# Performance work log

Measured on AMD Instinct MI355X. Metric: run time of the kernel, lower is better.

Reference implementation:

```python
import jax, jax.numpy as jnp
import numpy as np

DIM = 1024; HEADS = 16; HEAD = 64; FFN_H = 4096
LE = 8; TOPK = 2; DIM_E = 512; DIM_S = 1024
B = 1; S = 2048; N = B * S; NMOE = 2
THETA = 10000.0; EPS = 1e-6; RSF = 1.0


def rmsnorm(x, g):
    return x * jax.lax.rsqrt(jnp.mean(x * x, axis=-1, keepdims=True) + EPS) * g


def rotary(x):
    # x: [b, h, s, a]; matches RotaryEmb: split halves, y1=x1*cos+x2*sin, y2=-x1*sin+x2*cos
    a = x.shape[-1]; s = x.shape[2]
    inv_freq = (1.0 / THETA) ** (jnp.arange(0, a, 2, dtype=jnp.float32) / a)
    freqs = jnp.arange(s, dtype=jnp.float32)[:, None] * inv_freq[None, :]  # [s, a/2]
    cos, sin = jnp.cos(freqs), jnp.sin(freqs)
    x1, x2 = jnp.split(x, 2, axis=-1)
    return jnp.concatenate([x1 * cos + x2 * sin, -x1 * sin + x2 * cos], axis=-1)


def attention(x, attn_w, attn_o, doc):
    # causal + same-document masked attention (flex_attention mask_mod equivalent)
    b, s, d = x.shape
    xq, xk, xv = jnp.split(x @ attn_w, 3, axis=-1)
    def heads(t):
        return t.reshape(b, s, HEADS, HEAD).transpose(0, 2, 1, 3)
    xq, xk, xv = heads(xq), heads(xk), heads(xv)
    xq, xk = rotary(xq), rotary(xk)
    scores = jnp.einsum('bhqa,bhka->bhqk', xq, xk) / jnp.sqrt(jnp.float32(HEAD))
    q_idx = jnp.arange(s)
    mask = (q_idx[:, None] >= q_idx[None, :])[None] & (doc[:, :, None] == doc[:, None, :])
    scores = jnp.where(mask[:, None, :, :], scores, -jnp.inf)
    probs = jax.nn.softmax(scores, axis=-1)
    out = jnp.einsum('bhqk,bhka->bhqa', probs, xv)
    return out.transpose(0, 2, 1, 3).reshape(b, s, d) @ attn_o


def dense_layer(x, aw, ao, up, down, ag, fg, doc):
    xi = attention(rmsnorm(x, ag), aw, ao, doc) + x
    xf = rmsnorm(xi, fg)
    x1, x2 = jnp.split(xf @ up, 2, axis=-1)
    return (jax.nn.silu(x1) * x2) @ down + xi


def moe_layer(x, aw, ao, ag, fg, experts, tkeys, rbias, sup, sdown, idx, vals, doc):
    xi = attention(rmsnorm(x, ag), aw, ao, doc) + x
    xf = rmsnorm(xi, fg)                     # [b,s,d]
    flat = xf.reshape(-1, DIM)               # [N,d]
    # routing: base values + token-key logits + bias, sigmoid, renormalize
    tv = flat @ tkeys                        # [N,le]
    vals = vals + jnp.take_along_axis(tv, idx, axis=-1) + rbias[idx]
    sc = jax.nn.sigmoid(vals)
    sc = sc / jnp.sum(sc, axis=-1, keepdims=True) * RSF   # [N,k]
    # grouped-gemm experts (SwiGLU per expert); dense-over-experts then gather
    h1 = jnp.einsum('nd,edh->neh', flat, experts[0])
    h2 = jnp.einsum('nd,edh->neh', flat, experts[1])
    y_all = jnp.einsum('neh,edh->ned', jax.nn.silu(h1) * h2, experts[2])
    y_sel = jnp.take_along_axis(y_all, idx[:, :, None], axis=1)   # [N,k,d]
    y = jnp.sum(y_sel * sc[:, :, None], axis=1).reshape(xf.shape)
    # shared expert
    x1, x2 = jnp.split(xf @ sup, 2, axis=-1)
    y = y + (jax.nn.silu(x1) * x2) @ sdown
    return y + xi


def setup_inputs() -> dict:
    key = jax.random.key(0)
    ks = jax.random.split(key, 24)
    w = lambda k, shp: (jax.random.normal(k, shp, dtype=jnp.float32) * 0.02)
    inp = {
        'x': jax.random.normal(ks[0], (B, S, DIM), dtype=jnp.float32),
        'doc': jnp.sort(jax.random.randint(ks[1], (B, S), 0, 4), axis=-1).astype(jnp.int32),
        'indices': jax.random.randint(ks[2], (NMOE, N, TOPK), 0, LE).astype(jnp.int64),
        'values': jax.random.normal(ks[3], (NMOE, N, TOPK), dtype=jnp.float32),
        # 2 dense layers (first_k=1, last_k=1)
        'dense_attn_w': w(ks[4], (2, DIM, 3 * DIM)),
        'dense_attn_o': w(ks[5], (2, DIM, DIM)),
        'dense_ffn_up': w(ks[6], (2, DIM, 2 * FFN_H)),
        'dense_ffn_down': w(ks[7], (2, FFN_H, DIM)),
        'dense_attn_g': jnp.ones((2, DIM), dtype=jnp.float32),
        'dense_ffn_g': jnp.ones((2, DIM), dtype=jnp.float32),
        # 2 MoE layers
        'moe_attn_w': w(ks[8], (NMOE, DIM, 3 * DIM)),
        'moe_attn_o': w(ks[9], (NMOE, DIM, DIM)),
        'moe_attn_g': jnp.ones((NMOE, DIM), dtype=jnp.float32),
        'moe_ffn_g': jnp.ones((NMOE, DIM), dtype=jnp.float32),
        'moe_experts': w(ks[10], (NMOE, 3, LE, DIM, DIM_E)),
        'moe_token_keys': w(ks[11], (NMOE, DIM, LE)),
        'moe_router_bias': jnp.zeros((NMOE, LE), dtype=jnp.float32),
        'moe_shared_up': w(ks[12], (NMOE, DIM, 2 * DIM_S)),
        'moe_shared_down': w(ks[13], (NMOE, DIM_S, DIM)),
    }
    return inp


def reference(x, doc, indices, values, dense_attn_w, dense_attn_o, dense_ffn_up,
              dense_ffn_down, dense_attn_g, dense_ffn_g, moe_attn_w, moe_attn_o,
              moe_attn_g, moe_ffn_g, moe_experts, moe_token_keys, moe_router_bias,
              moe_shared_up, moe_shared_down):
    x = dense_layer(x, dense_attn_w[0], dense_attn_o[0], dense_ffn_up[0],
                    dense_ffn_down[0], dense_attn_g[0], dense_ffn_g[0], doc)
    for i in range(NMOE):
        x = moe_layer(x, moe_attn_w[i], moe_attn_o[i], moe_attn_g[i], moe_ffn_g[i],
                      moe_experts[i], moe_token_keys[i], moe_router_bias[i],
                      moe_shared_up[i], moe_shared_down[i], indices[i], values[i], doc)
    x = dense_layer(x, dense_attn_w[1], dense_attn_o[1], dense_ffn_up[1],
                    dense_ffn_down[1], dense_attn_g[1], dense_ffn_g[1], doc)
    return x
```

## Files before the change

kernel.cpp:

```cpp
#include <hip/hip_runtime.h>
#include <cmath>
#include <cstddef>
#include <cstdint>

#define DIMM   1024
#define HEADS  16
#define HEADD  64
#define FFN_H  4096
#define LE     8
#define TOPK   2
#define DIM_E  512
#define DIM_S  1024
#define NTOK   2048

typedef __bf16 bf16x8 __attribute__((ext_vector_type(8)));
typedef float  f32x4  __attribute__((ext_vector_type(4)));

union BF4 { __bf16 h[4]; uint2 u; };
union BF2 { __bf16 h[2]; uint32_t u; };

__device__ __forceinline__ void ldg_lds16(const __bf16* g, __bf16* l) {
    __builtin_amdgcn_global_load_lds(
        (const __attribute__((address_space(1))) uint32_t*)g,
        (__attribute__((address_space(3))) uint32_t*)l, 16, 0, 0);
}

__global__ __launch_bounds__(256) void rmsnorm_bf(
    const float* __restrict__ x, const float* __restrict__ g,
    __bf16* __restrict__ y)
{
    const int row = blockIdx.x;
    const int t = threadIdx.x;
    const float* xr = x + (size_t)row * DIMM;
    float4 v = *(const float4*)(xr + t * 4);
    float ss = v.x * v.x + v.y * v.y + v.z * v.z + v.w * v.w;
    #pragma unroll
    for (int off = 32; off > 0; off >>= 1) ss += __shfl_down(ss, off, 64);
    __shared__ float ws[4];
    if ((t & 63) == 0) ws[t >> 6] = ss;
    __syncthreads();
    const float tot = ws[0] + ws[1] + ws[2] + ws[3];
    const float scale = rsqrtf(tot * (1.0f / DIMM) + 1e-6f);
    const float4 gv = *(const float4*)(g + t * 4);
    BF4 o;
    o.h[0] = (__bf16)(v.x * scale * gv.x);
    o.h[1] = (__bf16)(v.y * scale * gv.y);
    o.h[2] = (__bf16)(v.z * scale * gv.z);
    o.h[3] = (__bf16)(v.w * scale * gv.w);
    *(uint2*)(y + (size_t)row * DIMM + t * 4) = o.u;
}

template <typename OutT>
__global__ __launch_bounds__(256) void gemm_bf_t(
    const __bf16* __restrict__ A, const __bf16* __restrict__ BT,
    const float* __restrict__ add, OutT* __restrict__ C,
    int M, int N, int K)
{
    __shared__ __bf16 As[128 * 32];
    __shared__ __bf16 Bs[128 * 32];
    const int t = threadIdx.x;
    const int m0 = blockIdx.y * 128, n0 = blockIdx.x * 128;
    const int lane = t & 63;
    const int wv = t >> 6;
    const int mw = (wv >> 1) * 64, nw = (wv & 1) * 64;
    const int fr = lane & 15;
    const int fk = (lane >> 4) * 8;
    const int r0 = t >> 2;
    const int q0 = (t & 3) * 8;

    const __bf16* gA0 = A + (size_t)(m0 + r0) * K + q0;
    const __bf16* gA1 = A + (size_t)(m0 + 64 + r0) * K + q0;
    const __bf16* gB0 = BT + (size_t)(n0 + r0) * K + q0;
    const __bf16* gB1 = BT + (size_t)(n0 + 64 + r0) * K + q0;
    __bf16* lA0 = &As[r0 * 32 + q0];
    __bf16* lA1 = &As[(64 + r0) * 32 + q0];
    __bf16* lB0 = &Bs[r0 * 32 + q0];
    __bf16* lB1 = &Bs[(64 + r0) * 32 + q0];

    f32x4 acc[4][4];
    #pragma unroll
    for (int i = 0; i < 4; ++i)
        #pragma unroll
        for (int j = 0; j < 4; ++j) acc[i][j] = (f32x4){0.f, 0.f, 0.f, 0.f};

    for (int k0 = 0; k0 < K; k0 += 32) {
        __syncthreads();
        ldg_lds16(gA0 + k0, lA0);
        ldg_lds16(gA1 + k0, lA1);
        ldg_lds16(gB0 + k0, lB0);
        ldg_lds16(gB1 + k0, lB1);
        __syncthreads();
        bf16x8 af[4], bfr[4];
        #pragma unroll
        for (int i = 0; i < 4; ++i) {
            af[i]  = *(const bf16x8*)&As[(mw + i * 16 + fr) * 32 + fk];
            bfr[i] = *(const bf16x8*)&Bs[(nw + i * 16 + fr) * 32 + fk];
        }
        #pragma unroll
        for (int i = 0; i < 4; ++i)
            #pragma unroll
            for (int j = 0; j < 4; ++j)
                acc[i][j] = __builtin_amdgcn_mfma_f32_16x16x32_bf16(
                    af[i], bfr[j], acc[i][j], 0, 0, 0);
    }
    const int cn = lane & 15, cr = (lane >> 4) * 4;
    #pragma unroll
    for (int i = 0; i < 4; ++i)
        #pragma unroll
        for (int j = 0; j < 4; ++j)
            #pragma unroll
            for (int r = 0; r < 4; ++r) {
                const size_t off = (size_t)(m0 + mw + i * 16 + cr + r) * N
                                 + (n0 + nw + j * 16 + cn);
                if constexpr (__is_same(OutT, float))
                    C[off] = acc[i][j][r] + (add ? add[off] : 0.f);
                else
                    C[off] = (__bf16)acc[i][j][r];
            }
}

__global__ __launch_bounds__(256) void gemm_bf_splitk(
    const __bf16* __restrict__ A, const __bf16* __restrict__ BT,
    float* __restrict__ P, int M, int N, int K, int KS)
{
    __shared__ __bf16 As[128 * 32];
    __shared__ __bf16 Bs[128 * 32];
    const int t = threadIdx.x;
    const int m0 = blockIdx.y * 128, n0 = blockIdx.x * 128;
    const int kz0 = blockIdx.z * KS;
    const int lane = t & 63;
    const int wv = t >> 6;
    const int mw = (wv >> 1) * 64, nw = (wv & 1) * 64;
    const int fr = lane & 15;
    const int fk = (lane >> 4) * 8;
    const int r0 = t >> 2;
    const int q0 = (t & 3) * 8;

    const __bf16* gA0 = A + (size_t)(m0 + r0) * K + q0;
    const __bf16* gA1 = A + (size_t)(m0 + 64 + r0) * K + q0;
    const __bf16* gB0 = BT + (size_t)(n0 + r0) * K + q0;
    const __bf16* gB1 = BT + (size_t)(n0 + 64 + r0) * K + q0;
    __bf16* lA0 = &As[r0 * 32 + q0];
    __bf16* lA1 = &As[(64 + r0) * 32 + q0];
    __bf16* lB0 = &Bs[r0 * 32 + q0];
    __bf16* lB1 = &Bs[(64 + r0) * 32 + q0];

    f32x4 acc[4][4];
    #pragma unroll
    for (int i = 0; i < 4; ++i)
        #pragma unroll
        for (int j = 0; j < 4; ++j) acc[i][j] = (f32x4){0.f, 0.f, 0.f, 0.f};

    for (int k0 = kz0; k0 < kz0 + KS; k0 += 32) {
        __syncthreads();
        ldg_lds16(gA0 + k0, lA0);
        ldg_lds16(gA1 + k0, lA1);
        ldg_lds16(gB0 + k0, lB0);
        ldg_lds16(gB1 + k0, lB1);
        __syncthreads();
        bf16x8 af[4], bfr[4];
        #pragma unroll
        for (int i = 0; i < 4; ++i) {
            af[i]  = *(const bf16x8*)&As[(mw + i * 16 + fr) * 32 + fk];
            bfr[i] = *(const bf16x8*)&Bs[(nw + i * 16 + fr) * 32 + fk];
        }
        #pragma unroll
        for (int i = 0; i < 4; ++i)
            #pragma unroll
            for (int j = 0; j < 4; ++j)
                acc[i][j] = __builtin_amdgcn_mfma_f32_16x16x32_bf16(
                    af[i], bfr[j], acc[i][j], 0, 0, 0);
    }
    float* Pz = P + (size_t)blockIdx.z * M * N;
    const int cn = lane & 15, cr = (lane >> 4) * 4;
    #pragma unroll
    for (int i = 0; i < 4; ++i)
        #pragma unroll
        for (int j = 0; j < 4; ++j)
            #pragma unroll
            for (int r = 0; r < 4; ++r) {
                const size_t off = (size_t)(m0 + mw + i * 16 + cr + r) * N
                                 + (n0 + nw + j * 16 + cn);
                Pz[off] = acc[i][j][r];
            }
}

__global__ __launch_bounds__(256) void reduce4_add(
    const float* __restrict__ P, const float* __restrict__ add,
    float* __restrict__ out, size_t MN)
{
    const size_t i = ((size_t)blockIdx.x * 256 + threadIdx.x) * 4;
    float4 s  = *(const float4*)(P + i);
    const float4 s1 = *(const float4*)(P + MN + i);
    const float4 s2 = *(const float4*)(P + 2 * MN + i);
    const float4 s3 = *(const float4*)(P + 3 * MN + i);
    const float4 a  = *(const float4*)(add + i);
    s.x += s1.x + s2.x + s3.x + a.x;
    s.y += s1.y + s2.y + s3.y + a.y;
    s.z += s1.z + s2.z + s3.z + a.z;
    s.w += s1.w + s2.w + s3.w + a.w;
    *(float4*)(out + i) = s;
}

__global__ __launch_bounds__(256) void transpose_cast(
    const float* __restrict__ in, __bf16* __restrict__ out, int R, int C)
{
    __shared__ float tile[32][33];
    const int bx = blockIdx.x * 32, by = blockIdx.y * 32;
    const size_t bz = (size_t)blockIdx.z * R * C;
    const int tx = threadIdx.x & 31, ty = threadIdx.x >> 5;
    const float* ip = in + bz;
    __bf16* op = out + bz;
    #pragma unroll
    for (int i = 0; i < 4; ++i)
        tile[ty + i * 8][tx] = ip[(size_t)(by + ty + i * 8) * C + bx + tx];
    __syncthreads();
    #pragma unroll
    for (int i = 0; i < 4; ++i)
        op[(size_t)(bx + ty + i * 8) * R + by + tx] = (__bf16)tile[tx][ty + i * 8];
}

__global__ __launch_bounds__(256) void cast_w2(
    const float* __restrict__ in, __bf16* __restrict__ out)
{
    const int i = blockIdx.x * 256 + threadIdx.x;
    const int d = i >> 12, r = i & 4095;
    const int e = r >> 9, h = r & 511;
    out[i] = (__bf16)in[(size_t)e * (DIMM * DIM_E) + d * DIM_E + h];
}

__global__ __launch_bounds__(256) void rotary_kernel(float* __restrict__ qkv)
{
    const int i = blockIdx.x * 256 + threadIdx.x;
    const int s = i >> 9;
    const int rem = i & 511;
    const int h = rem >> 5;
    const int j = rem & 31;
    const float inv_freq = __expf(-(float)j * (9.210340371976184f / 32.f));
    const float f = (float)s * inv_freq;
    float sn, cs;
    sincosf(f, &sn, &cs);
    float* base = qkv + (size_t)s * 3072 + h * 64 + j;
    const float q1 = base[0], q2 = base[32];
    base[0]  = q1 * cs + q2 * sn;
    base[32] = -q1 * sn + q2 * cs;
    const float k1 = base[1024], k2 = base[1024 + 32];
    base[1024]      = k1 * cs + k2 * sn;
    base[1024 + 32] = -k1 * sn + k2 * cs;
}

#define KS_STRIDE 72
#define VT_STRIDE 72
#define PW_STRIDE 36
#define LOG2E 1.4426950408889634f

__global__ __launch_bounds__(256) void attn_mfma(
    const float* __restrict__ qkv, const int* __restrict__ doc,
    __bf16* __restrict__ out)
{
    const int h = blockIdx.x;
    const int qb = blockIdx.y;
    const int t = threadIdx.x;
    const int wv = t >> 6, lane = t & 63;
    const int l15 = lane & 15, lhi = lane >> 4;
    const int q0w = qb * 64 + wv * 16;

    __shared__ __bf16 Ks[64 * KS_STRIDE];
    __shared__ __bf16 Vt[64 * VT_STRIDE];
    __shared__ float  Pw[4][16 * PW_STRIDE];
    __shared__ int    docs[64];

    bf16x8 qf[2];
    {
        const float* qrow = qkv + (size_t)(q0w + l15) * 3072 + h * 64 + lhi * 8;
        #pragma unroll
        for (int db = 0; db < 2; ++db) {
            const float4 v0 = *(const float4*)(qrow + db * 32);
            const float4 v1 = *(const float4*)(qrow + db * 32 + 4);
            bf16x8 f;
            f[0] = (__bf16)(v0.x * 0.125f); f[1] = (__bf16)(v0.y * 0.125f);
            f[2] = (__bf16)(v0.z * 0.125f); f[3] = (__bf16)(v0.w * 0.125f);
            f[4] = (__bf16)(v1.x * 0.125f); f[5] = (__bf16)(v1.y * 0.125f);
            f[6] = (__bf16)(v1.z * 0.125f); f[7] = (__bf16)(v1.w * 0.125f);
            qf[db] = f;
        }
    }
    int myDoc[4];
    #pragma unroll
    for (int rg = 0; rg < 4; ++rg) myDoc[rg] = doc[q0w + lhi * 4 + rg];

    float mrow[4] = {-INFINITY, -INFINITY, -INFINITY, -INFINITY};
    float lrow[4] = {0.f, 0.f, 0.f, 0.f};
    f32x4 oacc[4];
    #pragma unroll
    for (int nb = 0; nb < 4; ++nb) oacc[nb] = (f32x4){0.f, 0.f, 0.f, 0.f};

    const int docQ0 = doc[qb * 64];
    const int ntiles = qb + 1;

    for (int kt = 0; kt < ntiles; ++kt) {
        if (doc[kt * 64 + 63] < docQ0) continue;
        __syncthreads();
        {
            const int key = t >> 2, dof = (t & 3) * 16;
            const float* kr = qkv + (size_t)(kt * 64 + key) * 3072 + 1024 + h * 64 + dof;
            float kv[16];
            *(float4*)&kv[0]  = *(const float4*)(kr + 0);
            *(float4*)&kv[4]  = *(const float4*)(kr + 4);
            *(float4*)&kv[8]  = *(const float4*)(kr + 8);
            *(float4*)&kv[12] = *(const float4*)(kr + 12);
            bf16x8 p0, p1;
            #pragma unroll
            for (int j = 0; j < 8; ++j) { p0[j] = (__bf16)kv[j]; p1[j] = (__bf16)kv[8 + j]; }
            *(bf16x8*)&Ks[key * KS_STRIDE + dof] = p0;
            *(bf16x8*)&Ks[key * KS_STRIDE + dof + 8] = p1;
            const int k2 = (t & 31) * 2, df = (t >> 5) * 8;
            const float* vr0 = qkv + (size_t)(kt * 64 + k2) * 3072 + 2048 + h * 64 + df;
            float va[8], vb[8];
            *(float4*)&va[0] = *(const float4*)(vr0 + 0);
            *(float4*)&va[4] = *(const float4*)(vr0 + 4);
            *(float4*)&vb[0] = *(const float4*)(vr0 + 3072);
            *(float4*)&vb[4] = *(const float4*)(vr0 + 3076);
            #pragma unroll
            for (int d = 0; d < 8; ++d) {
                BF2 wpk;
                wpk.h[0] = (__bf16)va[d];
                wpk.h[1] = (__bf16)vb[d];
                *(uint32_t*)&Vt[(df + d) * VT_STRIDE + k2] = wpk.u;
            }
            if (t < 64) docs[t] = doc[kt * 64 + t];
        }
        __syncthreads();

        #pragma unroll
        for (int g = 0; g < 2; ++g) {
            f32x4 s[2];
            #pragma unroll
            for (int sg = 0; sg < 2; ++sg) {
                const int keyloc = g * 32 + sg * 16;
                const bf16x8 kf0 = *(const bf16x8*)&Ks[(keyloc + l15) * KS_STRIDE + lhi * 8];
                const bf16x8 kf1 = *(const bf16x8*)&Ks[(keyloc + l15) * KS_STRIDE + 32 + lhi * 8];
                f32x4 a = (f32x4){0.f, 0.f, 0.f, 0.f};
                a = __builtin_amdgcn_mfma_f32_16x16x32_bf16(qf[0], kf0, a, 0, 0, 0);
                a = __builtin_amdgcn_mfma_f32_16x16x32_bf16(qf[1], kf1, a, 0, 0, 0);
                s[sg] = a;
            }
            float sv0[4], sv1[4], cmax[4];
            #pragma unroll
            for (int rg = 0; rg < 4; ++rg) {
                const int r = q0w + lhi * 4 + rg;
                const int key0 = kt * 64 + g * 32 + l15;
                const bool v0 = (key0 <= r) && (docs[g * 32 + l15] == myDoc[rg]);
                const bool v1 = (key0 + 16 <= r) && (docs[g * 32 + 16 + l15] == myDoc[rg]);
                sv0[rg] = v0 ? s[0][rg] : -INFINITY;
                sv1[rg] = v1 ? s[1][rg] : -INFINITY;
                cmax[rg] = fmaxf(sv0[rg], sv1[rg]);
            }
            #pragma unroll
            for (int off = 1; off < 16; off <<= 1)
                #pragma unroll
                for (int rg = 0; rg < 4; ++rg)
                    cmax[rg] = fmaxf(cmax[rg], __shfl_xor(cmax[rg], off, 64));
            float alpha[4], p0[4], p1[4], rsum[4];
            #pragma unroll
            for (int rg = 0; rg < 4; ++rg) {
                const float mn = fmaxf(mrow[rg], cmax[rg]);
                alpha[rg] = (mn == -INFINITY) ? 1.f : exp2f((mrow[rg] - mn) * LOG2E);
                p0[rg] = (sv0[rg] == -INFINITY) ? 0.f : exp2f((sv0[rg] - mn) * LOG2E);
                p1[rg] = (sv1[rg] == -INFINITY) ? 0.f : exp2f((sv1[rg] - mn) * LOG2E);
                rsum[rg] = p0[rg] + p1[rg];
                mrow[rg] = mn;
            }
            #pragma unroll
            for (int off = 1; off < 16; off <<= 1)
                #pragma unroll
                for (int rg = 0; rg < 4; ++rg)
                    rsum[rg] += __shfl_xor(rsum[rg], off, 64);
            #pragma unroll
            for (int rg = 0; rg < 4; ++rg)
                lrow[rg] = lrow[rg] * alpha[rg] + rsum[rg];
            #pragma unroll
            for (int nb = 0; nb < 4; ++nb)
                #pragma unroll
                for (int rg = 0; rg < 4; ++rg)
                    oacc[nb][rg] *= alpha[rg];
            float* pp = &Pw[wv][0];
            #pragma unroll
            for (int rg = 0; rg < 4; ++rg) {
                pp[(lhi * 4 + rg) * PW_STRIDE + l15] = p0[rg];
                pp[(lhi * 4 + rg) * PW_STRIDE + 16 + l15] = p1[rg];
            }
            const f32x4 pa = *(const f32x4*)&pp[l15 * PW_STRIDE + lhi * 8];
            const f32x4 pb = *(const f32x4*)&pp[l15 * PW_STRIDE + lhi * 8 + 4];
            bf16x8 pf;
            pf[0] = (__bf16)pa[0]; pf[1] = (__bf16)pa[1];
            pf[2] = (__bf16)pa[2]; pf[3] = (__bf16)pa[3];
            pf[4] = (__bf16)pb[0]; pf[5] = (__bf16)pb[1];
            pf[6] = (__bf16)pb[2]; pf[7] = (__bf16)pb[3];
            #pragma unroll
            for (int nb = 0; nb < 4; ++nb) {
                const bf16x8 vf = *(const bf16x8*)&Vt[(nb * 16 + l15) * VT_STRIDE + g * 32 + lhi * 8];
                oacc[nb] = __builtin_amdgcn_mfma_f32_16x16x32_bf16(pf, vf, oacc[nb], 0, 0, 0);
            }
        }
    }
    float inv[4];
    #pragma unroll
    for (int rg = 0; rg < 4; ++rg) inv[rg] = 1.f / lrow[rg];
    #pragma unroll
    for (int nb = 0; nb < 4; ++nb)
        #pragma unroll
        for (int rg = 0; rg < 4; ++rg)
            out[(size_t)(q0w + lhi * 4 + rg) * DIMM + h * 64 + nb * 16 + l15] =
                (__bf16)(oacc[nb][rg] * inv[rg]);
}

__global__ __launch_bounds__(256) void swiglu_bf2(
    const __bf16* __restrict__ h, __bf16* __restrict__ g, int shift)
{
    const int i4 = blockIdx.x * 256 + threadIdx.x;
    const int H = 1 << shift;
    const int n = (i4 * 4) >> shift;
    const int j = (i4 * 4) & (H - 1);
    const __bf16* hr = h + ((size_t)n << (shift + 1));
    BF4 a, b;
    a.u = *(const uint2*)(hr + j);
    b.u = *(const uint2*)(hr + H + j);
    BF4 o;
    #pragma unroll
    for (int u = 0; u < 4; ++u) {
        const float av = (float)a.h[u], bv = (float)b.h[u];
        o.h[u] = (__bf16)((av / (1.f + __expf(-av))) * bv);
    }
    *(uint2*)(g + (size_t)i4 * 4) = o.u;
}

__global__ __launch_bounds__(256) void pmask_bf2(
    const __bf16* __restrict__ hh, const float* __restrict__ sc,
    __bf16* __restrict__ p)
{
    const int i4 = blockIdx.x * 256 + threadIdx.x;
    const int n = i4 >> 10;
    const int j4 = i4 & 1023;
    const int e = j4 >> 7;
    const float s = sc[n * LE + e];
    const __bf16* hr = hh + (size_t)n * 8192 + j4 * 4;
    BF4 a, b;
    a.u = *(const uint2*)(hr);
    b.u = *(const uint2*)(hr + 4096);
    BF4 o;
    #pragma unroll
    for (int u = 0; u < 4; ++u) {
        const float av = (float)a.h[u], bv = (float)b.h[u];
        o.h[u] = (__bf16)((av / (1.f + __expf(-av))) * bv * s);
    }
    *(uint2*)(p + (size_t)i4 * 4) = o.u;
}

__global__ __launch_bounds__(64) void router_bf(
    const __bf16* __restrict__ xf, const float* __restrict__ tkeys,
    const float* __restrict__ rbias, const int* __restrict__ idx,
    const float* __restrict__ vals, float* __restrict__ sc)
{
    const int n = blockIdx.x;
    const int t = threadIdx.x;
    const int e0 = idx[n * 2 + 0], e1 = idx[n * 2 + 1];
    float a0 = 0.f, a1 = 0.f;
    for (int d = t; d < DIMM; d += 64) {
        const float xv = (float)xf[(size_t)n * DIMM + d];
        a0 += xv * tkeys[d * LE + e0];
        a1 += xv * tkeys[d * LE + e1];
    }
    #pragma unroll
    for (int off = 32; off > 0; off >>= 1) {
        a0 += __shfl_down(a0, off, 64);
        a1 += __shfl_down(a1, off, 64);
    }
    if (t == 0) {
        const float v0 = vals[n * 2 + 0] + a0 + rbias[e0];
        const float v1 = vals[n * 2 + 1] + a1 + rbias[e1];
        const float s0 = 1.f / (1.f + __expf(-v0));
        const float s1 = 1.f / (1.f + __expf(-v1));
        const float inv = 1.f / (s0 + s1);
        float r[LE];
        #pragma unroll
        for (int e = 0; e < LE; ++e) r[e] = 0.f;
        r[e0] += s0 * inv;
        r[e1] += s1 * inv;
        #pragma unroll
        for (int e = 0; e < LE; ++e) sc[n * LE + e] = r[e];
    }
}

struct Scratch {
    float *qkv, *xi, *t1, *sc, *xA, *xB, *part;
    __bf16 *xn_bf, *attnO_bf, *xf_bf, *wbuf, *gact_bf, *gs_bf, *hh_bf, *hs_bf;
};

static void attn_block(const float* x_in, const __bf16* awT, const __bf16* aoT,
                       const float* ag, const int* doc, Scratch& w, hipStream_t s)
{
    rmsnorm_bf<<<NTOK, 256, 0, s>>>(x_in, ag, w.xn_bf);
    gemm_bf_t<float><<<dim3(24, 16), 256, 0, s>>>(w.xn_bf, awT, nullptr, w.qkv, NTOK, 3072, 1024);
    rotary_kernel<<<(NTOK * 512) / 256, 256, 0, s>>>(w.qkv);
    attn_mfma<<<dim3(HEADS, NTOK / 64), 256, 0, s>>>(w.qkv, doc, w.attnO_bf);
    gemm_bf_t<float><<<dim3(8, 16), 256, 0, s>>>(w.attnO_bf, aoT, x_in, w.xi, NTOK, 1024, 1024);
}

static void dense_layer_run(const float* x_in, float* x_out,
                            const float* aw, const float* ao,
                            const float* up, const float* down,
                            const float* ag, const float* fg,
                            const int* doc, Scratch& w, hipStream_t s)
{
    __bf16* awT = w.wbuf;
    __bf16* aoT = w.wbuf + 3145728;
    __bf16* upT = w.wbuf + 4194304;
    __bf16* dnT = w.wbuf + 12582912;
    transpose_cast<<<dim3(96, 32, 1), 256, 0, s>>>(aw, awT, 1024, 3072);
    transpose_cast<<<dim3(32, 32, 1), 256, 0, s>>>(ao, aoT, 1024, 1024);
    transpose_cast<<<dim3(256, 32, 1), 256, 0, s>>>(up, upT, 1024, 8192);
    transpose_cast<<<dim3(32, 128, 1), 256, 0, s>>>(down, dnT, 4096, 1024);
    attn_block(x_in, awT, aoT, ag, doc, w, s);
    rmsnorm_bf<<<NTOK, 256, 0, s>>>(w.xi, fg, w.xf_bf);
    gemm_bf_t<__bf16><<<dim3(64, 16), 256, 0, s>>>(w.xf_bf, upT, nullptr, w.hh_bf, NTOK, 8192, 1024);
    swiglu_bf2<<<(NTOK * FFN_H / 4) / 256, 256, 0, s>>>(w.hh_bf, w.gact_bf, 12);
    gemm_bf_splitk<<<dim3(8, 16, 4), 256, 0, s>>>(w.gact_bf, dnT, w.part, NTOK, 1024, 4096, 1024);
    reduce4_add<<<(NTOK * 1024) / 1024, 256, 0, s>>>(w.part, w.xi, x_out, (size_t)NTOK * 1024);
}

static void moe_layer_run(const float* x_in, float* x_out,
                          const float* aw, const float* ao,
                          const float* ag, const float* fg,
                          const float* experts, const float* tkeys,
                          const float* rbias, const float* sup,
                          const float* sdn, const int* idx, const float* vals,
                          const int* doc, Scratch& w, hipStream_t s)
{
    __bf16* awT  = w.wbuf;
    __bf16* aoT  = w.wbuf + 3145728;
    __bf16* w01T = w.wbuf + 4194304;
    __bf16* w2c  = w.wbuf + 12582912;
    __bf16* supT = w.wbuf + 16777216;
    __bf16* sdnT = w.wbuf + 18874368;
    const size_t EW = (size_t)LE * DIMM * DIM_E;
    transpose_cast<<<dim3(96, 32, 1), 256, 0, s>>>(aw, awT, 1024, 3072);
    transpose_cast<<<dim3(32, 32, 1), 256, 0, s>>>(ao, aoT, 1024, 1024);
    transpose_cast<<<dim3(16, 32, 8), 256, 0, s>>>(experts, w01T, 1024, 512);
    transpose_cast<<<dim3(16, 32, 8), 256, 0, s>>>(experts + EW, w01T + 4194304, 1024, 512);
    cast_w2<<<16384, 256, 0, s>>>(experts + 2 * EW, w2c);
    transpose_cast<<<dim3(64, 32, 1), 256, 0, s>>>(sup, supT, 1024, 2048);
    transpose_cast<<<dim3(32, 32, 1), 256, 0, s>>>(sdn, sdnT, 1024, 1024);

    attn_block(x_in, awT, aoT, ag, doc, w, s);
    rmsnorm_bf<<<NTOK, 256, 0, s>>>(w.xi, fg, w.xf_bf);
    router_bf<<<NTOK, 64, 0, s>>>(w.xf_bf, tkeys, rbias, idx, vals, w.sc);
    gemm_bf_t<__bf16><<<dim3(64, 16), 256, 0, s>>>(w.xf_bf, w01T, nullptr, w.hh_bf, NTOK, 8192, 1024);
    pmask_bf2<<<(NTOK * 4096 / 4) / 256, 256, 0, s>>>(w.hh_bf, w.sc, w.gact_bf);
    gemm_bf_t<__bf16><<<dim3(16, 16), 256, 0, s>>>(w.xf_bf, supT, nullptr, w.hs_bf, NTOK, 2048, 1024);
    swiglu_bf2<<<(NTOK * DIM_S / 4) / 256, 256, 0, s>>>(w.hs_bf, w.gs_bf, 10);
    gemm_bf_t<float><<<dim3(8, 16), 256, 0, s>>>(w.gs_bf, sdnT, w.xi, w.t1, NTOK, 1024, 1024);
    gemm_bf_splitk<<<dim3(8, 16, 4), 256, 0, s>>>(w.gact_bf, w2c, w.part, NTOK, 1024, 4096, 1024);
    reduce4_add<<<(NTOK * 1024) / 1024, 256, 0, s>>>(w.part, w.t1, x_out, (size_t)NTOK * 1024);
}

extern "C" void kernel_launch(void* const* d_in, const int* in_sizes, int n_in,
                              void* d_out, int out_size, void* d_ws, size_t ws_size,
                              hipStream_t stream)
{
    (void)in_sizes; (void)n_in; (void)out_size; (void)ws_size;
    const float* x       = (const float*)d_in[0];
    const int*   doc     = (const int*)d_in[1];
    const int*   indices = (const int*)d_in[2];
    const float* values  = (const float*)d_in[3];
    const float* d_aw    = (const float*)d_in[4];
    const float* d_ao    = (const float*)d_in[5];
    const float* d_up    = (const float*)d_in[6];
    const float* d_down  = (const float*)d_in[7];
    const float* d_ag    = (const float*)d_in[8];
    const float* d_fg    = (const float*)d_in[9];
    const float* m_aw    = (const float*)d_in[10];
    const float* m_ao    = (const float*)d_in[11];
    const float* m_ag    = (const float*)d_in[12];
    const float* m_fg    = (const float*)d_in[13];
    const float* m_ex    = (const float*)d_in[14];
    const float* m_tk    = (const float*)d_in[15];
    const float* m_rb    = (const float*)d_in[16];
    const float* m_sup   = (const float*)d_in[17];
    const float* m_sdn   = (const float*)d_in[18];

    Scratch w;
    float* f = (float*)d_ws;
    w.qkv = f; f += 6291456;
    w.xi  = f; f += 2097152;
    float* h12 = f; f += 16777216;
    w.t1  = h12 + 8388608;
    w.sc  = f; f += 16384;
    w.xA  = f; f += 2097152;
    w.xB  = f; f += 2097152;
    __bf16* b = (__bf16*)f;
    w.xn_bf    = b; b += 2097152;
    w.attnO_bf = b; b += 2097152;
    w.xf_bf    = b; b += 2097152;
    w.wbuf     = b; b += 19922944;
    w.gact_bf  = (__bf16*)w.qkv;
    w.gs_bf    = (__bf16*)w.qkv + 8388608;
    w.hh_bf    = (__bf16*)h12;
    w.hs_bf    = (__bf16*)(h12 + 8388608 + 2097152);
    w.part     = h12;

    float* out = (float*)d_out;

    dense_layer_run(x, w.xA, d_aw, d_ao, d_up, d_down, d_ag, d_fg, doc, w, stream);
    const size_t EXL = (size_t)3 * LE * DIMM * DIM_E;
    moe_layer_run(w.xA, w.xB,
                  m_aw, m_ao, m_ag, m_fg,
                  m_ex, m_tk, m_rb, m_sup, m_sdn,
                  indices, values, doc, w, stream);
    moe_layer_run(w.xB, w.xA,
                  m_aw + (size_t)DIMM * 3 * DIMM, m_ao + (size_t)DIMM * DIMM,
                  m_ag + DIMM, m_fg + DIMM,
                  m_ex + EXL, m_tk + DIMM * LE, m_rb + LE,
                  m_sup + (size_t)DIMM * 2 * DIM_S, m_sdn + (size_t)DIM_S * DIMM,
                  indices + (size_t)NTOK * TOPK, values + (size_t)NTOK * TOPK,
                  doc, w, stream);
    dense_layer_run(w.xA, out,
                    d_aw + (size_t)DIMM * 3 * DIMM, d_ao + (size_t)DIMM * DIMM,
                    d_up + (size_t)DIMM * 2 * FFN_H, d_down + (size_t)FFN_H * DIMM,
                    d_ag + DIMM, d_fg + DIMM, doc, w, stream);
}
```

Baseline: 1.437 ms.

## Fuse SwiGLU into up-projection GEMM, swizzle LDS, split-K small GEMMs

Adds a gemm_glu kernel that loads paired gate/up weight rows into one tile and applies SiLU-gate (and router scale) in the epilogue, removing the separate swiglu/pmask passes and the intermediate bf16 hidden buffers. GEMM kernels get an XOR swizzle on LDS columns to reduce bank conflicts on fragment reads. The N=1024,K=1024 output projections switch to 2-way split-K plus a reduce kernel to raise block count. This adds an extra fp32 partial buffer round trip for those GEMMs.

```diff
diff --git a/kernel.cpp b/kernel.cpp
--- a/kernel.cpp
+++ b/kernel.cpp
@@ -64,18 +64,19 @@
     const int wv = t >> 6;
     const int mw = (wv >> 1) * 64, nw = (wv & 1) * 64;
     const int fr = lane & 15;
-    const int fk = (lane >> 4) * 8;
+    const int fk = ((lane >> 4) ^ ((fr >> 1) & 3)) * 8;
     const int r0 = t >> 2;
-    const int q0 = (t & 3) * 8;
-
-    const __bf16* gA0 = A + (size_t)(m0 + r0) * K + q0;
-    const __bf16* gA1 = A + (size_t)(m0 + 64 + r0) * K + q0;
-    const __bf16* gB0 = BT + (size_t)(n0 + r0) * K + q0;
-    const __bf16* gB1 = BT + (size_t)(n0 + 64 + r0) * K + q0;
-    __bf16* lA0 = &As[r0 * 32 + q0];
-    __bf16* lA1 = &As[(64 + r0) * 32 + q0];
-    __bf16* lB0 = &Bs[r0 * 32 + q0];
-    __bf16* lB1 = &Bs[(64 + r0) * 32 + q0];
+    const int q0l = (t & 3) * 8;
+    const int q0s = ((t & 3) ^ ((t >> 3) & 3)) * 8;
+
+    const __bf16* gA0 = A + (size_t)(m0 + r0) * K + q0s;
+    const __bf16* gA1 = A + (size_t)(m0 + 64 + r0) * K + q0s;
+    const __bf16* gB0 = BT + (size_t)(n0 + r0) * K + q0s;
+    const __bf16* gB1 = BT + (size_t)(n0 + 64 + r0) * K + q0s;
+    __bf16* lA0 = &As[r0 * 32 + q0l];
+    __bf16* lA1 = &As[(64 + r0) * 32 + q0l];
+    __bf16* lB0 = &Bs[r0 * 32 + q0l];
+    __bf16* lB1 = &Bs[(64 + r0) * 32 + q0l];
 
     f32x4 acc[4][4];
     #pragma unroll
@@ -132,18 +133,19 @@
     const int wv = t >> 6;
     const int mw = (wv >> 1) * 64, nw = (wv & 1) * 64;
     const int fr = lane & 15;
-    const int fk = (lane >> 4) * 8;
+    const int fk = ((lane >> 4) ^ ((fr >> 1) & 3)) * 8;
     const int r0 = t >> 2;
-    const int q0 = (t & 3) * 8;
-
-    const __bf16* gA0 = A + (size_t)(m0 + r0) * K + q0;
-    const __bf16* gA1 = A + (size_t)(m0 + 64 + r0) * K + q0;
-    const __bf16* gB0 = BT + (size_t)(n0 + r0) * K + q0;
-    const __bf16* gB1 = BT + (size_t)(n0 + 64 + r0) * K + q0;
-    __bf16* lA0 = &As[r0 * 32 + q0];
-    __bf16* lA1 = &As[(64 + r0) * 32 + q0];
-    __bf16* lB0 = &Bs[r0 * 32 + q0];
-    __bf16* lB1 = &Bs[(64 + r0) * 32 + q0];
+    const int q0l = (t & 3) * 8;
+    const int q0s = ((t & 3) ^ ((t >> 3) & 3)) * 8;
+
+    const __bf16* gA0 = A + (size_t)(m0 + r0) * K + q0s;
+    const __bf16* gA1 = A + (size_t)(m0 + 64 + r0) * K + q0s;
+    const __bf16* gB0 = BT + (size_t)(n0 + r0) * K + q0s;
+    const __bf16* gB1 = BT + (size_t)(n0 + 64 + r0) * K + q0s;
+    __bf16* lA0 = &As[r0 * 32 + q0l];
+    __bf16* lA1 = &As[(64 + r0) * 32 + q0l];
+    __bf16* lB0 = &Bs[r0 * 32 + q0l];
+    __bf16* lB1 = &Bs[(64 + r0) * 32 + q0l];
 
     f32x4 acc[4][4];
     #pragma unroll
@@ -183,6 +185,83 @@
                                  + (n0 + nw + j * 16 + cn);
                 Pz[off] = acc[i][j][r];
             }
+}
+
+__global__ __launch_bounds__(256) void gemm_glu(
+    const __bf16* __restrict__ A, const __bf16* __restrict__ BT,
+    const float* __restrict__ sc, __bf16* __restrict__ G,
+    int M, int Nout, int K, int pairOff)
+{
+    __shared__ __bf16 As[128 * 32];
+    __shared__ __bf16 Bs[128 * 32];
+    const int t = threadIdx.x;
+    const int m0 = blockIdx.y * 128;
+    const int b  = blockIdx.x;
+    const int lane = t & 63;
+    const int wv = t >> 6;
+    const int mw = (wv >> 1) * 64, nw = (wv & 1) * 64;
+    const int fr = lane & 15;
+    const int fk = ((lane >> 4) ^ ((fr >> 1) & 3)) * 8;
+    const int r0 = t >> 2;
+    const int q0l = (t & 3) * 8;
+    const int q0s = ((t & 3) ^ ((t >> 3) & 3)) * 8;
+
+    const int grow0 = b * 64 + ((r0 >> 6) ? 32 : 0) + (r0 & 31)
+                    + ((r0 >> 5) & 1) * pairOff;
+    const int grow1 = grow0 + 32;
+
+    const __bf16* gA0 = A + (size_t)(m0 + r0) * K + q0s;
+    const __bf16* gA1 = A + (size_t)(m0 + 64 + r0) * K + q0s;
+    const __bf16* gB0 = BT + (size_t)grow0 * K + q0s;
+    const __bf16* gB1 = BT + (size_t)grow1 * K + q0s;
+    __bf16* lA0 = &As[r0 * 32 + q0l];
+    __bf16* lA1 = &As[(64 + r0) * 32 + q0l];
+    __bf16* lB0 = &Bs[r0 * 32 + q0l];
+    __bf16* lB1 = &Bs[(64 + r0) * 32 + q0l];
+
+    f32x4 acc[4][4];
+    #pragma unroll
+    for (int i = 0; i < 4; ++i)
+        #pragma unroll
+        for (int j = 0; j < 4; ++j) acc[i][j] = (f32x4){0.f, 0.f, 0.f, 0.f};
+
+    for (int k0 = 0; k0 < K; k0 += 32) {
+        __syncthreads();
+        ldg_lds16(gA0 + k0, lA0);
+        ldg_lds16(gA1 + k0, lA1);
+        ldg_lds16(gB0 + k0, lB0);
+        ldg_lds16(gB1 + k0, lB1);
+        __syncthreads();
+        bf16x8 af[4], bfr[4];
+        #pragma unroll
+        for (int i = 0; i < 4; ++i) {
+            af[i]  = *(const bf16x8*)&As[(mw + i * 16 + fr) * 32 + fk];
+            bfr[i] = *(const bf16x8*)&Bs[(nw + i * 16 + fr) * 32 + fk];
+        }
+        #pragma unroll
+        for (int i = 0; i < 4; ++i)
+            #pragma unroll
+            for (int j = 0; j < 4; ++j)
+                acc[i][j] = __builtin_amdgcn_mfma_f32_16x16x32_bf16(
+                    af[i], bfr[j], acc[i][j], 0, 0, 0);
+    }
+    const int cn = lane & 15, cr = (lane >> 4) * 4;
+    const int e = (b * 64) >> 9;
+    #pragma unroll
+    for (int i = 0; i < 4; ++i)
+        #pragma unroll
+        for (int r = 0; r < 4; ++r) {
+            const int m = m0 + mw + i * 16 + cr + r;
+            const float s = sc ? sc[m * LE + e] : 1.f;
+            #pragma unroll
+            for (int j = 0; j < 2; ++j) {
+                const float h1 = acc[i][j][r];
+                const float h2 = acc[i][j + 2][r];
+                const float o = (h1 / (1.f + __expf(-h1))) * h2 * s;
+                const int col = b * 64 + (nw >> 1) + j * 16 + cn;
+                G[(size_t)m * Nout + col] = (__bf16)o;
+            }
+        }
 }
 
 __global__ __launch_bounds__(256) void reduce4_add(
@@ -199,6 +278,21 @@
     s.y += s1.y + s2.y + s3.y + a.y;
     s.z += s1.z + s2.z + s3.z + a.z;
     s.w += s1.w + s2.w + s3.w + a.w;
+    *(float4*)(out + i) = s;
+}
+
+__global__ __launch_bounds__(256) void reduce2_add(
+    const float* __restrict__ P, const float* __restrict__ add,
+    float* __restrict__ out, size_t MN)
+{
+    const size_t i = ((size_t)blockIdx.x * 256 + threadIdx.x) * 4;
+    float4 s  = *(const float4*)(P + i);
+    const float4 s1 = *(const float4*)(P + MN + i);
+    const float4 a  = *(const float4*)(add + i);
+    s.x += s1.x + a.x;
+    s.y += s1.y + a.y;
+    s.z += s1.z + a.z;
+    s.w += s1.w + a.w;
     *(float4*)(out + i) = s;
 }
 
@@ -415,48 +509,6 @@
                 (__bf16)(oacc[nb][rg] * inv[rg]);
 }
 
-__global__ __launch_bounds__(256) void swiglu_bf2(
-    const __bf16* __restrict__ h, __bf16* __restrict__ g, int shift)
-{
-    const int i4 = blockIdx.x * 256 + threadIdx.x;
-    const int H = 1 << shift;
-    const int n = (i4 * 4) >> shift;
-    const int j = (i4 * 4) & (H - 1);
-    const __bf16* hr = h + ((size_t)n << (shift + 1));
-    BF4 a, b;
-    a.u = *(const uint2*)(hr + j);
-    b.u = *(const uint2*)(hr + H + j);
-    BF4 o;
-    #pragma unroll
-    for (int u = 0; u < 4; ++u) {
-        const float av = (float)a.h[u], bv = (float)b.h[u];
-        o.h[u] = (__bf16)((av / (1.f + __expf(-av))) * bv);
-    }
-    *(uint2*)(g + (size_t)i4 * 4) = o.u;
-}
-
-__global__ __launch_bounds__(256) void pmask_bf2(
-    const __bf16* __restrict__ hh, const float* __restrict__ sc,
-    __bf16* __restrict__ p)
-{
-    const int i4 = blockIdx.x * 256 + threadIdx.x;
-    const int n = i4 >> 10;
-    const int j4 = i4 & 1023;
-    const int e = j4 >> 7;
-    const float s = sc[n * LE + e];
-    const __bf16* hr = hh + (size_t)n * 8192 + j4 * 4;
-    BF4 a, b;
-    a.u = *(const uint2*)(hr);
-    b.u = *(const uint2*)(hr + 4096);
-    BF4 o;
-    #pragma unroll
-    for (int u = 0; u < 4; ++u) {
-        const float av = (float)a.h[u], bv = (float)b.h[u];
-        o.h[u] = (__bf16)((av / (1.f + __expf(-av))) * bv * s);
-    }
-    *(uint2*)(p + (size_t)i4 * 4) = o.u;
-}
-
 __global__ __launch_bounds__(64) void router_bf(
     const __bf16* __restrict__ xf, const float* __restrict__ tkeys,
     const float* __restrict__ rbias, const int* __restrict__ idx,
@@ -494,7 +546,7 @@
 
 struct Scratch {
     float *qkv, *xi, *t1, *sc, *xA, *xB, *part;
-    __bf16 *xn_bf, *attnO_bf, *xf_bf, *wbuf, *gact_bf, *gs_bf, *hh_bf, *hs_bf;
+    __bf16 *xn_bf, *attnO_bf, *xf_bf, *wbuf, *gact_bf, *gs_bf;
 };
 
 static void attn_block(const float* x_in, const __bf16* awT, const __bf16* aoT,
@@ -504,7 +556,8 @@
     gemm_bf_t<float><<<dim3(24, 16), 256, 0, s>>>(w.xn_bf, awT, nullptr, w.qkv, NTOK, 3072, 1024);
     rotary_kernel<<<(NTOK * 512) / 256, 256, 0, s>>>(w.qkv);
     attn_mfma<<<dim3(HEADS, NTOK / 64), 256, 0, s>>>(w.qkv, doc, w.attnO_bf);
-    gemm_bf_t<float><<<dim3(8, 16), 256, 0, s>>>(w.attnO_bf, aoT, x_in, w.xi, NTOK, 1024, 1024);
+    gemm_bf_splitk<<<dim3(8, 16, 2), 256, 0, s>>>(w.attnO_bf, aoT, w.qkv, NTOK, 1024, 1024, 512);
+    reduce2_add<<<(NTOK * 1024) / 1024, 256, 0, s>>>(w.qkv, x_in, w.xi, (size_t)NTOK * 1024);
 }
 
 static void dense_layer_run(const float* x_in, float* x_out,
@@ -523,8 +576,7 @@
     transpose_cast<<<dim3(32, 128, 1), 256, 0, s>>>(down, dnT, 4096, 1024);
     attn_block(x_in, awT, aoT, ag, doc, w, s);
     rmsnorm_bf<<<NTOK, 256, 0, s>>>(w.xi, fg, w.xf_bf);
-    gemm_bf_t<__bf16><<<dim3(64, 16), 256, 0, s>>>(w.xf_bf, upT, nullptr, w.hh_bf, NTOK, 8192, 1024);
-    swiglu_bf2<<<(NTOK * FFN_H / 4) / 256, 256, 0, s>>>(w.hh_bf, w.gact_bf, 12);
+    gemm_glu<<<dim3(64, 16), 256, 0, s>>>(w.xf_bf, upT, nullptr, w.gact_bf, NTOK, 4096, 1024, 4096);
     gemm_bf_splitk<<<dim3(8, 16, 4), 256, 0, s>>>(w.gact_bf, dnT, w.part, NTOK, 1024, 4096, 1024);
     reduce4_add<<<(NTOK * 1024) / 1024, 256, 0, s>>>(w.part, w.xi, x_out, (size_t)NTOK * 1024);
 }
@@ -555,11 +607,10 @@
     attn_block(x_in, awT, aoT, ag, doc, w, s);
     rmsnorm_bf<<<NTOK, 256, 0, s>>>(w.xi, fg, w.xf_bf);
     router_bf<<<NTOK, 64, 0, s>>>(w.xf_bf, tkeys, rbias, idx, vals, w.sc);
-    gemm_bf_t<__bf16><<<dim3(64, 16), 256, 0, s>>>(w.xf_bf, w01T, nullptr, w.hh_bf, NTOK, 8192, 1024);
-    pmask_bf2<<<(NTOK * 4096 / 4) / 256, 256, 0, s>>>(w.hh_bf, w.sc, w.gact_bf);
-    gemm_bf_t<__bf16><<<dim3(16, 16), 256, 0, s>>>(w.xf_bf, supT, nullptr, w.hs_bf, NTOK, 2048, 1024);
-    swiglu_bf2<<<(NTOK * DIM_S / 4) / 256, 256, 0, s>>>(w.hs_bf, w.gs_bf, 10);
-    gemm_bf_t<float><<<dim3(8, 16), 256, 0, s>>>(w.gs_bf, sdnT, w.xi, w.t1, NTOK, 1024, 1024);
+    gemm_glu<<<dim3(64, 16), 256, 0, s>>>(w.xf_bf, w01T, w.sc, w.gact_bf, NTOK, 4096, 1024, 4096);
+    gemm_glu<<<dim3(16, 16), 256, 0, s>>>(w.xf_bf, supT, nullptr, w.gs_bf, NTOK, 1024, 1024, 1024);
+    gemm_bf_splitk<<<dim3(8, 16, 2), 256, 0, s>>>(w.gs_bf, sdnT, w.part, NTOK, 1024, 1024, 512);
+    reduce2_add<<<(NTOK * 1024) / 1024, 256, 0, s>>>(w.part, w.xi, w.t1, (size_t)NTOK * 1024);
     gemm_bf_splitk<<<dim3(8, 16, 4), 256, 0, s>>>(w.gact_bf, w2c, w.part, NTOK, 1024, 4096, 1024);
     reduce4_add<<<(NTOK * 1024) / 1024, 256, 0, s>>>(w.part, w.t1, x_out, (size_t)NTOK * 1024);
 }
@@ -605,8 +656,6 @@
     w.wbuf     = b; b += 19922944;
     w.gact_bf  = (__bf16*)w.qkv;
     w.gs_bf    = (__bf16*)w.qkv + 8388608;
-    w.hh_bf    = (__bf16*)h12;
-    w.hs_bf    = (__bf16*)(h12 + 8388608 + 2097152);
     w.part     = h12;
 
     float* out = (float*)d_out;
```

Result: faster. 1.325 ms (-7.8%).
